# Performance work log

Measured on AMD Instinct MI355X. Metric: run time of the kernel, lower is better.

Reference implementation:

```python
import jax, jax.numpy as jnp
import numpy as np

HIDDEN = 1024
BATCH = 32
SRC_LEN = 2048
NEG_BIG = -1e10


def setup_inputs() -> dict:
    key = jax.random.key(0)
    k1, k2, k3, k4, k5, k6 = jax.random.split(key, 6)
    s = 1.0 / np.sqrt(2 * HIDDEN)
    return {
        "decoder_hidden": jax.random.normal(k1, (BATCH, HIDDEN), dtype=jnp.float32),
        "encoder_outputs": jax.random.normal(k2, (BATCH, SRC_LEN, HIDDEN), dtype=jnp.float32),
        "mask": jax.random.randint(k3, (BATCH, SRC_LEN), 0, 2, dtype=jnp.int32),
        # attn: Linear(2H -> H). Store as (2H, H) so x @ W matches torch x @ W.T
        "attn_W": jax.random.uniform(k4, (2 * HIDDEN, HIDDEN), jnp.float32, -s, s),
        "attn_b": jax.random.uniform(k5, (HIDDEN,), jnp.float32, -s, s),
        # v: Linear(H -> 1, bias=False), stored as (H,)
        "v_w": jax.random.uniform(k6, (HIDDEN,), jnp.float32, -1.0 / np.sqrt(HIDDEN), 1.0 / np.sqrt(HIDDEN)),
    }


def reference(decoder_hidden, encoder_outputs, mask, attn_W, attn_b, v_w):
    # Split the concat-linear: [dec, enc] @ W == dec @ W_dec + enc @ W_enc (same math, no big concat)
    W_dec, W_enc = attn_W[:HIDDEN], attn_W[HIDDEN:]
    dec_proj = decoder_hidden @ W_dec + attn_b            # (B, H)
    enc_proj = jnp.einsum("bsh,hk->bsk", encoder_outputs, W_enc)  # (B, S, H)
    energy = jnp.tanh(dec_proj[:, None, :] + enc_proj)    # (B, S, H)
    attention = jnp.einsum("bsh,h->bs", energy, v_w)      # (B, S)
    attention = jnp.where(mask == 0, NEG_BIG, attention)
    attention_weights = jax.nn.softmax(attention, axis=1)  # (B, S)
    context = jnp.einsum("bs,bsh->bh", attention_weights, encoder_outputs)  # (B, H)
    return attention_weights, context
```

## Files before the change

kernel.cpp:

```cpp
#include <hip/hip_runtime.h>
#include <hip/hip_bf16.h>
#include <math.h>

#define HIDDEN 1024
#define BATCH 32
#define SRC_LEN 2048
#define NROWS (BATCH * SRC_LEN)
#define NEG_BIG -10000000000.0f

typedef __attribute__((ext_vector_type(8))) short bf16x8;
typedef __attribute__((ext_vector_type(4))) float f32x4;
typedef __attribute__((ext_vector_type(16))) float f32x16;
typedef __attribute__((ext_vector_type(4))) unsigned uint32x4;

static __device__ __forceinline__ unsigned short f2bf(float f) {
  unsigned u = __float_as_uint(f);
  u = u + 0x7fffu + ((u >> 16) & 1u);
  return (unsigned short)(u >> 16);
}

static __device__ __forceinline__ unsigned cvtpk(float lo, float hi) {
  unsigned r;
  asm("v_cvt_pk_bf16_f32 %0, %1, %2" : "=v"(r) : "v"(lo), "v"(hi));
  return r;
}

static __device__ __forceinline__ void gload16(const void* g, void* l) {
  __builtin_amdgcn_global_load_lds(
      reinterpret_cast<const __attribute__((address_space(1))) unsigned*>(
          reinterpret_cast<unsigned long long>(g)),
      reinterpret_cast<__attribute__((address_space(3))) unsigned*>(
          reinterpret_cast<unsigned long long>(l)),
      16, 0, 0);
}

__global__ __launch_bounds__(256) void k_wt(
    const float* __restrict__ W, unsigned short* __restrict__ WT) {
  __shared__ float ts[64][65];
  const int hy = blockIdx.y * 64, nx = blockIdx.x * 64;
  const int tid = threadIdx.x;
#pragma unroll
  for (int i = 0; i < 16; ++i) {
    int idx = tid + i * 256, r = idx >> 6, c = idx & 63;
    ts[r][c] = W[(HIDDEN + hy + r) * HIDDEN + nx + c];
  }
  __syncthreads();
#pragma unroll
  for (int i = 0; i < 16; ++i) {
    int idx = tid + i * 256, rn = idx >> 6, ch = idx & 63;
    WT[(nx + rn) * HIDDEN + hy + ch] = f2bf(ts[ch][rn]);
  }
}

__global__ __launch_bounds__(256) void k_dec_part(
    const float* __restrict__ dh, const float* __restrict__ W,
    float* __restrict__ decpart) {
  const int kl = threadIdx.x & 63;
  const int bq = threadIdx.x >> 6;
  const int k = blockIdx.x * 64 + kl;
  const int h0 = blockIdx.y * 64;
  __shared__ float dh_s[64][33];
#pragma unroll
  for (int i = 0; i < 8; ++i) {
    int idx = threadIdx.x + i * 256;
    int b = idx >> 6, hh = idx & 63;
    dh_s[hh][b] = dh[b * HIDDEN + h0 + hh];
  }
  __syncthreads();
  float acc[8] = {0.f, 0.f, 0.f, 0.f, 0.f, 0.f, 0.f, 0.f};
#pragma unroll
  for (int hh = 0; hh < 64; ++hh) {
    float w = W[(h0 + hh) * HIDDEN + k];
#pragma unroll
    for (int bb = 0; bb < 8; ++bb) acc[bb] += dh_s[hh][bq * 8 + bb] * w;
  }
#pragma unroll
  for (int bb = 0; bb < 8; ++bb)
    decpart[blockIdx.y * (BATCH * HIDDEN) + (bq * 8 + bb) * HIDDEN + k] = acc[bb];
}

__global__ __launch_bounds__(256) void k_dec_reduce(
    const float* __restrict__ decpart, const float* __restrict__ bias,
    float* __restrict__ out) {
  int e = blockIdx.x * 256 + threadIdx.x;
  float s = bias[e & (HIDDEN - 1)];
#pragma unroll
  for (int hc = 0; hc < 16; ++hc) s += decpart[hc * (BATCH * HIDDEN) + e];
  out[e] = s;
}

#define BM 256
#define BN 256
#define BK 64
#define NT (HIDDEN / BK)

__global__ __launch_bounds__(512, 2) void k_energy_mfma(
    const float* __restrict__ enc, const unsigned short* __restrict__ WT,
    const float* __restrict__ dec_proj, const float* __restrict__ v_w,
    float* __restrict__ part) {
  __shared__ unsigned short As[2][BM * BK];
  __shared__ unsigned short Bs[2][BN * BK];
  __shared__ float red[4][BM];

  const int tid = threadIdx.x;
  const int lane = tid & 63;
  const int wid = tid >> 6;
  const int wm = wid >> 2;
  const int wn = wid & 3;
  const int c31 = lane & 31;
  const int hi = lane >> 5;

  const int bid = blockIdx.x;
  const int l = (bid & 7) * 128 + (bid >> 3);
  const int n0 = (l & 3) * BN;
  const int row0 = (l >> 2) * BM;
  const int b = row0 >> 11;

  f32x16 acc[4][2];
#pragma unroll
  for (int m = 0; m < 4; ++m)
#pragma unroll
    for (int n = 0; n < 2; ++n)
#pragma unroll
      for (int e = 0; e < 16; ++e) acc[m][n][e] = 0.f;

  const float4* enc4 = (const float4*)enc;

  const int rbase = tid >> 3;
  const int c16 = tid & 7;
  const float4* ea = enc4 + (size_t)(row0 + rbase) * 256 + c16 * 2;
  const unsigned aswz = ((unsigned)(rbase & 7)) << 4;
  const unsigned awoff = (unsigned)rbase * 128 + (((unsigned)c16 * 16) ^ aswz);

  const char* wb = (const char*)WT +
                   (size_t)(n0 + wid * 8 + (lane >> 3)) * 2048 +
                   ((((unsigned)(lane & 7)) * 16) ^ (((unsigned)(lane >> 3)) << 4));
  const unsigned bldsoff = (unsigned)wid * 1024;

  float4 pa[4][2];

#define STAGE_ISSUE(tile, pdst)                                            \
  do {                                                                     \
    _Pragma("unroll") for (int i = 0; i < 4; ++i)                          \
        gload16(wb + (size_t)i * 131072 + (size_t)(tile) * 128,            \
                (char*)Bs[pdst] + bldsoff + i * 8192);                     \
    _Pragma("unroll") for (int i = 0; i < 4; ++i) {                        \
      pa[i][0] = ea[(size_t)i * 16384 + (tile) * 16];                      \
      pa[i][1] = ea[(size_t)i * 16384 + (tile) * 16 + 1];                  \
    }                                                                      \
  } while (0)

#define STAGE_WRITE(pdst)                                                  \
  do {                                                                     \
    _Pragma("unroll") for (int i = 0; i < 4; ++i) {                        \
      uint32x4 q;                                                          \
      q.x = cvtpk(pa[i][0].x, pa[i][0].y);                                 \
      q.y = cvtpk(pa[i][0].z, pa[i][0].w);                                 \
      q.z = cvtpk(pa[i][1].x, pa[i][1].y);                                 \
      q.w = cvtpk(pa[i][1].z, pa[i][1].w);                                 \
      *(uint32x4*)((char*)As[pdst] + awoff + i * 8192) = q;                \
    }                                                                      \
  } while (0)

#define MFMA_STEP(p)                                                       \
  do {                                                                     \
    _Pragma("unroll") for (int ks = 0; ks < 4; ++ks) {                     \
      bf16x8 af[4], bv[2];                                                 \
      const unsigned koff = (unsigned)(ks * 32 + hi * 16);                 \
      _Pragma("unroll") for (int mt = 0; mt < 4; ++mt) {                   \
        int r = wm * 128 + mt * 32 + c31;                                  \
        unsigned off = (unsigned)r * 128 +                                 \
                       (koff ^ (((unsigned)(r & 7)) << 4));                \
        af[mt] = *(const bf16x8*)((const char*)As[p] + off);               \
      }                                                                    \
      _Pragma("unroll") for (int nt = 0; nt < 2; ++nt) {                   \
        int c = wn * 64 + nt * 32 + c31;                                   \
        unsigned off = (unsigned)c * 128 +                                 \
                       (koff ^ (((unsigned)(c & 7)) << 4));                \
        bv[nt] = *(const bf16x8*)((const char*)Bs[p] + off);               \
      }                                                                    \
      __builtin_amdgcn_s_setprio(1);                                       \
      _Pragma("unroll") for (int mt = 0; mt < 4; ++mt)                     \
          _Pragma("unroll") for (int nt = 0; nt < 2; ++nt)                 \
              acc[mt][nt] = __builtin_amdgcn_mfma_f32_32x32x16_bf16(       \
                  af[mt], bv[nt], acc[mt][nt], 0, 0, 0);                   \
      __builtin_amdgcn_s_setprio(0);                                       \
    }                                                                      \
  } while (0)

#define STEP(tt, p)                                                        \
  do {                                                                     \
    if ((tt) + 1 < NT) STAGE_ISSUE((tt) + 1, (p) ^ 1);                     \
    MFMA_STEP(p);                                                          \
    if ((tt) + 1 < NT) STAGE_WRITE((p) ^ 1);                               \
    __syncthreads();                                                       \
  } while (0)

  STAGE_ISSUE(0, 0);
  STAGE_WRITE(0);
  __syncthreads();

  for (int t = 0; t < NT; t += 2) {
    STEP(t, 0);
    STEP(t + 1, 1);
  }

  float dv[2], vv[2];
#pragma unroll
  for (int nt = 0; nt < 2; ++nt) {
    int kc = n0 + wn * 64 + nt * 32 + c31;
    dv[nt] = dec_proj[b * HIDDEN + kc];
    vv[nt] = v_w[kc];
  }
#pragma unroll
  for (int mt = 0; mt < 4; ++mt) {
#pragma unroll
    for (int reg = 0; reg < 16; ++reg) {
      float p = 0.f;
#pragma unroll
      for (int nt = 0; nt < 2; ++nt) {
        float x = dv[nt] + acc[mt][nt][reg];
        float t = 1.f - 2.f / (__expf(2.f * x) + 1.f);
        p += t * vv[nt];
      }
      p += __shfl_xor(p, 1);
      p += __shfl_xor(p, 2);
      p += __shfl_xor(p, 4);
      p += __shfl_xor(p, 8);
      p += __shfl_xor(p, 16);
      if (c31 == 0) {
        int row = wm * 128 + mt * 32 + (reg & 3) + 8 * (reg >> 2) + 4 * hi;
        red[wn][row] = p;
      }
    }
  }
  __syncthreads();
  if (tid < BM) {
    float s = red[0][tid] + red[1][tid] + red[2][tid] + red[3][tid];
    part[(size_t)(l & 3) * NROWS + row0 + tid] = s;
  }
#undef STAGE_ISSUE
#undef STAGE_WRITE
#undef MFMA_STEP
#undef STEP
}

__global__ __launch_bounds__(256) void k_softmax(
    const float* __restrict__ part, const int* __restrict__ mask,
    float* __restrict__ out_w) {
  int b = blockIdx.x, tid = threadIdx.x;
  __shared__ float red[4], red2[4];
  float l[8];
  float m = -INFINITY;
#pragma unroll
  for (int j = 0; j < 8; ++j) {
    int s = tid + 256 * j;
    int row = b * SRC_LEN + s;
    float x = part[row] + part[NROWS + row] + part[2 * NROWS + row] +
              part[3 * NROWS + row];
    l[j] = (mask[row] == 0) ? NEG_BIG : x;
    m = fmaxf(m, l[j]);
  }
#pragma unroll
  for (int off = 32; off; off >>= 1) m = fmaxf(m, __shfl_xor(m, off));
  if ((tid & 63) == 0) red[tid >> 6] = m;
  __syncthreads();
  m = fmaxf(fmaxf(red[0], red[1]), fmaxf(red[2], red[3]));
  float sum = 0.f;
#pragma unroll
  for (int j = 0; j < 8; ++j) {
    l[j] = expf(l[j] - m);
    sum += l[j];
  }
#pragma unroll
  for (int off = 32; off; off >>= 1) sum += __shfl_xor(sum, off);
  if ((tid & 63) == 0) red2[tid >> 6] = sum;
  __syncthreads();
  sum = red2[0] + red2[1] + red2[2] + red2[3];
  float inv = 1.f / sum;
#pragma unroll
  for (int j = 0; j < 8; ++j) out_w[b * SRC_LEN + tid + 256 * j] = l[j] * inv;
}

__global__ __launch_bounds__(256) void k_ctx_partial(
    const float* __restrict__ w, const float* __restrict__ enc,
    float* __restrict__ part) {
  int b = blockIdx.x, sg = blockIdx.y, tid = threadIdx.x;
  const float4* enc4 = (const float4*)enc;
  float4 acc = {0.f, 0.f, 0.f, 0.f};
  int s0 = sg * 128;
#pragma unroll 4
  for (int s = 0; s < 128; ++s) {
    float ws = w[b * SRC_LEN + s0 + s];
    float4 e = enc4[(size_t)(b * SRC_LEN + s0 + s) * 256 + tid];
    acc.x += ws * e.x;
    acc.y += ws * e.y;
    acc.z += ws * e.z;
    acc.w += ws * e.w;
  }
  ((float4*)part)[(b * 16 + sg) * 256 + tid] = acc;
}

__global__ __launch_bounds__(256) void k_ctx_reduce(
    const float* __restrict__ part, float* __restrict__ ctx) {
  int b = blockIdx.x, tid = threadIdx.x;
  float4 acc = {0.f, 0.f, 0.f, 0.f};
#pragma unroll
  for (int sg = 0; sg < 16; ++sg) {
    float4 p = ((const float4*)part)[(b * 16 + sg) * 256 + tid];
    acc.x += p.x;
    acc.y += p.y;
    acc.z += p.z;
    acc.w += p.w;
  }
  ((float4*)ctx)[b * 256 + tid] = acc;
}

extern "C" void kernel_launch(void* const* d_in, const int* in_sizes, int n_in,
                              void* d_out, int out_size, void* d_ws, size_t ws_size,
                              hipStream_t stream) {
  const float* dh = (const float*)d_in[0];
  const float* enc = (const float*)d_in[1];
  const int* mask = (const int*)d_in[2];
  const float* attn_W = (const float*)d_in[3];
  const float* attn_b = (const float*)d_in[4];
  const float* v_w = (const float*)d_in[5];

  float* out_w = (float*)d_out;
  float* out_ctx = (float*)d_out + NROWS;

  float* ws = (float*)d_ws;
  float* part = ws;
  float* dec_proj = ws + 4 * NROWS;
  float* ctxpart = dec_proj + BATCH * HIDDEN;
  float* decpart = ctxpart + BATCH * 16 * HIDDEN;
  unsigned short* WT = (unsigned short*)(decpart + 16 * BATCH * HIDDEN);

  k_wt<<<dim3(16, 16), 256, 0, stream>>>(attn_W, WT);
  k_dec_part<<<dim3(16, 16), 256, 0, stream>>>(dh, attn_W, decpart);
  k_dec_reduce<<<dim3(128), 256, 0, stream>>>(decpart, attn_b, dec_proj);
  k_energy_mfma<<<dim3(1024), 512, 0, stream>>>(enc, WT, dec_proj, v_w, part);
  k_softmax<<<dim3(BATCH), 256, 0, stream>>>(part, mask, out_w);
  k_ctx_partial<<<dim3(BATCH, 16), 256, 0, stream>>>(out_w, enc, ctxpart);
  k_ctx_reduce<<<dim3(BATCH), 256, 0, stream>>>(ctxpart, out_ctx);
}
```

Baseline: 260.7 us.

## Use k-chunked interleaved LDS and WT layout instead of XOR swizzle

Changes the transposed weight buffer to a layout grouped in 8-element k-chunks, so each row's 16-byte chunk for a given k-group is contiguous across n. The shared-memory A and B tiles are restructured the same way, with k-group-major, row-minor 16-byte slots. This removes the XOR swizzle arithmetic from the MFMA operand loads and makes each lane's global encoder load cover a contiguous half-row. The risk is less coalesced global reads of the encoder (each thread reads 128 contiguous bytes) and possible LDS bank conflicts in the new write pattern.

```diff
diff --git a/kernel.cpp b/kernel.cpp
--- a/kernel.cpp
+++ b/kernel.cpp
@@ -48,7 +48,8 @@
 #pragma unroll
   for (int i = 0; i < 16; ++i) {
     int idx = tid + i * 256, rn = idx >> 6, ch = idx & 63;
-    WT[(nx + rn) * HIDDEN + hy + ch] = f2bf(ts[ch][rn]);
+    int h = hy + ch, n = nx + rn;
+    WT[((size_t)(h >> 3) * 1024 + n) * 8 + (h & 7)] = f2bf(ts[ch][rn]);
   }
 }
 
@@ -126,59 +127,50 @@
 
   const float4* enc4 = (const float4*)enc;
 
-  const int rbase = tid >> 3;
-  const int c16 = tid & 7;
-  const float4* ea = enc4 + (size_t)(row0 + rbase) * 256 + c16 * 2;
-  const unsigned aswz = ((unsigned)(rbase & 7)) << 4;
-  const unsigned awoff = (unsigned)rbase * 128 + (((unsigned)c16 * 16) ^ aswz);
-
-  const char* wb = (const char*)WT +
-                   (size_t)(n0 + wid * 8 + (lane >> 3)) * 2048 +
-                   ((((unsigned)(lane & 7)) * 16) ^ (((unsigned)(lane >> 3)) << 4));
+  const int rbase = tid >> 1;
+  const int hhalf = tid & 1;
+  const float4* ea = enc4 + (size_t)(row0 + rbase) * 256 + hhalf * 8;
+  const unsigned awbase = (unsigned)hhalf * 16384 + (unsigned)rbase * 16;
+
+  const char* wbt = (const char*)WT +
+      ((size_t)(wid >> 2) * 1024 + (size_t)(n0 + (wid & 3) * 64 + lane)) * 16;
   const unsigned bldsoff = (unsigned)wid * 1024;
 
-  float4 pa[4][2];
+  float4 pa[8];
 
 #define STAGE_ISSUE(tile, pdst)                                            \
   do {                                                                     \
+    _Pragma("unroll") for (int j = 0; j < 8; ++j)                          \
+        pa[j] = ea[(size_t)(tile) * 16 + j];                               \
     _Pragma("unroll") for (int i = 0; i < 4; ++i)                          \
-        gload16(wb + (size_t)i * 131072 + (size_t)(tile) * 128,            \
+        gload16(wbt + (size_t)(tile) * 131072 + (size_t)i * 32768,         \
                 (char*)Bs[pdst] + bldsoff + i * 8192);                     \
-    _Pragma("unroll") for (int i = 0; i < 4; ++i) {                        \
-      pa[i][0] = ea[(size_t)i * 16384 + (tile) * 16];                      \
-      pa[i][1] = ea[(size_t)i * 16384 + (tile) * 16 + 1];                  \
+  } while (0)
+
+#define STAGE_WRITE(pdst)                                                  \
+  do {                                                                     \
+    _Pragma("unroll") for (int j = 0; j < 4; ++j) {                        \
+      uint32x4 qv;                                                         \
+      qv.x = cvtpk(pa[2 * j].x, pa[2 * j].y);                              \
+      qv.y = cvtpk(pa[2 * j].z, pa[2 * j].w);                              \
+      qv.z = cvtpk(pa[2 * j + 1].x, pa[2 * j + 1].y);                      \
+      qv.w = cvtpk(pa[2 * j + 1].z, pa[2 * j + 1].w);                      \
+      *(uint32x4*)((char*)As[pdst] + awbase + j * 4096) = qv;              \
     }                                                                      \
   } while (0)
 
-#define STAGE_WRITE(pdst)                                                  \
-  do {                                                                     \
-    _Pragma("unroll") for (int i = 0; i < 4; ++i) {                        \
-      uint32x4 q;                                                          \
-      q.x = cvtpk(pa[i][0].x, pa[i][0].y);                                 \
-      q.y = cvtpk(pa[i][0].z, pa[i][0].w);                                 \
-      q.z = cvtpk(pa[i][1].x, pa[i][1].y);                                 \
-      q.w = cvtpk(pa[i][1].z, pa[i][1].w);                                 \
-      *(uint32x4*)((char*)As[pdst] + awoff + i * 8192) = q;                \
-    }                                                                      \
-  } while (0)
-
 #define MFMA_STEP(p)                                                       \
   do {                                                                     \
+    const char* abase = (const char*)As[p] + (unsigned)hi * 4096 +         \
+                        ((unsigned)(wm * 128 + c31)) * 16;                 \
+    const char* bbase = (const char*)Bs[p] + (unsigned)hi * 4096 +         \
+                        ((unsigned)(wn * 64 + c31)) * 16;                  \
     _Pragma("unroll") for (int ks = 0; ks < 4; ++ks) {                     \
       bf16x8 af[4], bv[2];                                                 \
-      const unsigned koff = (unsigned)(ks * 32 + hi * 16);                 \
-      _Pragma("unroll") for (int mt = 0; mt < 4; ++mt) {                   \
-        int r = wm * 128 + mt * 32 + c31;                                  \
-        unsigned off = (unsigned)r * 128 +                                 \
-                       (koff ^ (((unsigned)(r & 7)) << 4));                \
-        af[mt] = *(const bf16x8*)((const char*)As[p] + off);               \
-      }                                                                    \
-      _Pragma("unroll") for (int nt = 0; nt < 2; ++nt) {                   \
-        int c = wn * 64 + nt * 32 + c31;                                   \
-        unsigned off = (unsigned)c * 128 +                                 \
-                       (koff ^ (((unsigned)(c & 7)) << 4));                \
-        bv[nt] = *(const bf16x8*)((const char*)Bs[p] + off);               \
-      }                                                                    \
+      _Pragma("unroll") for (int mt = 0; mt < 4; ++mt)                     \
+          af[mt] = *(const bf16x8*)(abase + ks * 8192 + mt * 512);         \
+      _Pragma("unroll") for (int nt = 0; nt < 2; ++nt)                     \
+          bv[nt] = *(const bf16x8*)(bbase + ks * 8192 + nt * 512);         \
       __builtin_amdgcn_s_setprio(1);                                       \
       _Pragma("unroll") for (int mt = 0; mt < 4; ++mt)                     \
           _Pragma("unroll") for (int nt = 0; nt < 2; ++nt)                 \
```

New measurement: 311.7 us. 19.6% more time.
